# Kernel optimization log

Hardware: AMD Instinct MI355X
Metric: run time of the kernel (lower is better)

## Reference

```python
import jax, jax.numpy as jnp
import numpy as np

B, S, A, H, E = 8192, 256, 64, 1024, 8
IN = S + A
OUT = S + 1


def setup_inputs() -> dict:
    key = jax.random.key(0)
    ks = jax.random.split(key, 8)
    state = jax.random.normal(ks[0], (B, S), dtype=jnp.float32)
    action = jax.random.normal(ks[1], (B, A), dtype=jnp.float32)
    idx = jax.random.randint(ks[2], (B,), 0, E, dtype=jnp.int32)
    # Kaiming-ish scaling to keep activations sane
    W1 = jax.random.normal(ks[3], (E, IN, H), dtype=jnp.float32) / np.sqrt(IN)
    b1 = jnp.zeros((E, H), dtype=jnp.float32)
    W2 = jax.random.normal(ks[4], (E, H, H), dtype=jnp.float32) / np.sqrt(H)
    b2 = jnp.zeros((E, H), dtype=jnp.float32)
    W3 = jax.random.normal(ks[5], (E, H, OUT), dtype=jnp.float32) / np.sqrt(H)
    b3 = jnp.zeros((E, OUT), dtype=jnp.float32)
    return {"state": state, "action": action, "idx": idx,
            "W1": W1, "b1": b1, "W2": W2, "b2": b2, "W3": W3, "b3": b3}


def reference(state, action, idx, W1, b1, W2, b2, W3, b3):
    # Dense-MoE style: run all E experts on the full batch, then select the
    # per-sample expert output chosen by idx (matches masked gather/scatter
    # in the torch predict loop).
    x = jnp.concatenate([state, action], axis=-1)                  # [B, IN]
    h = jax.nn.relu(jnp.einsum('bi,eih->beh', x, W1) + b1)         # [B, E, H]
    h = jax.nn.relu(jnp.einsum('beh,ehk->bek', h, W2) + b2)        # [B, E, H]
    out = jnp.einsum('beh,eho->beo', h, W3) + b3                   # [B, E, S+1]
    sel = jnp.take_along_axis(out, idx[:, None, None], axis=1)[:, 0]  # [B, S+1]
    s_dim = state.shape[-1]
    delta = sel[:, :s_dim]
    reward = sel[:, s_dim:]
    next_state = state + delta
    return next_state, reward
```

## Files before the change

### kernel.cpp

```cpp
#include <hip/hip_runtime.h>
#include <stdint.h>

#define B_SZ   8192
#define IN_DIM 320
#define H_DIM  1024
#define E_NUM  8
#define OUT_DIM 257
#define TM     128
#define MAXT   (B_SZ / TM + E_NUM)

typedef __bf16 bf16x8 __attribute__((ext_vector_type(8)));
typedef float  f32x4  __attribute__((ext_vector_type(4)));

typedef unsigned int __attribute__((address_space(1))) as1_uint;
typedef unsigned int __attribute__((address_space(3))) as3_uint;

__device__ __forceinline__ void gload_lds16(const void* g, void* l) {
    __builtin_amdgcn_global_load_lds((const as1_uint*)g, (as3_uint*)l, 16, 0, 0);
}

__device__ __forceinline__ unsigned short f2bf(float f) {
    unsigned int u = __float_as_uint(f);
    return (unsigned short)((u + 0x7fffu + ((u >> 16) & 1u)) >> 16);
}

__global__ __launch_bounds__(256)
void k_prep(const float* __restrict__ state, const float* __restrict__ action,
            const int* __restrict__ idx,
            const float* __restrict__ W1, const float* __restrict__ W2,
            const float* __restrict__ W3,
            unsigned short* __restrict__ xb, unsigned short* __restrict__ w1t,
            unsigned short* __restrict__ w2t, unsigned short* __restrict__ w3t,
            int* __restrict__ order, int* __restrict__ te,
            int* __restrict__ tp0, int* __restrict__ tcnt) {
    __shared__ unsigned short tileU[64][65];
    __shared__ int scnt[16][E_NUM];
    int bid = blockIdx.x, tid = threadIdx.x;

    if (bid == 0) {
        int shard = tid & 15;
        if (tid < 128) ((int*)scnt)[tid] = 0;
        __syncthreads();
        for (int b = tid; b < B_SZ; b += 256) atomicAdd(&scnt[shard][idx[b]], 1);
        __syncthreads();
        if (tid == 0) {
            int pos = 0, tt = 0;
            for (int e = 0; e < E_NUM; e++) {
                int start = pos;
                for (int s = 0; s < 16; s++) { int c = scnt[s][e]; scnt[s][e] = pos; pos += c; }
                int tot = pos - start;
                for (int st = 0; st < tot; st += TM) {
                    te[tt] = e; tp0[tt] = start + st; tcnt[tt] = min(TM, tot - st); tt++;
                }
            }
            for (; tt < MAXT; tt++) { te[tt] = 0; tp0[tt] = 0; tcnt[tt] = 0; }
        }
        __syncthreads();
        for (int b = tid; b < B_SZ; b += 256) {
            int e = idx[b];
            int p = atomicAdd(&scnt[shard][e], 1);
            order[p] = b;
        }
        return;
    }

    if (bid <= 2560) {
        int q = (bid - 1) * 256 + tid;
        int b = q / 80, j = q % 80;
        float4 v = (j < 64) ? ((const float4*)state)[b * 64 + j]
                            : ((const float4*)action)[b * 16 + (j - 64)];
        ushort4 o;
        o.x = f2bf(v.x); o.y = f2bf(v.y); o.z = f2bf(v.z); o.w = f2bf(v.w);
        ((ushort4*)xb)[q] = o;
        return;
    }

    if (bid < 5761) {
        int e, kt, nt, K, Nsrc, dstRows; bool vec;
        const float* src; unsigned short* dst;
        if (bid < 3201) {
            int r = bid - 2561; e = r / 80; int m = r % 80; kt = m / 16; nt = m % 16;
            K = IN_DIM; Nsrc = H_DIM; dstRows = H_DIM; src = W1; dst = w1t; vec = true;
        } else if (bid < 5249) {
            int r = bid - 3201; e = r / 256; int m = r % 256; kt = m / 16; nt = m % 16;
            K = H_DIM; Nsrc = H_DIM; dstRows = H_DIM; src = W2; dst = w2t; vec = true;
        } else {
            int r = bid - 5249; e = r / 64; int m = r % 64; kt = m / 4; nt = m % 4;
            K = H_DIM; Nsrc = OUT_DIM; dstRows = 320; src = W3; dst = w3t; vec = false;
        }
        int k0 = kt * 64, n0 = nt * 64;
        const float* s = src + (size_t)e * K * Nsrc;
        unsigned short* d = dst + (size_t)e * dstRows * K;
        int c4 = (tid & 15) * 4;
        int rb = tid >> 4;

#pragma unroll
        for (int p = 0; p < 4; p++) {
            int r = rb + p * 16;
            const float* sp = s + (size_t)(k0 + r) * Nsrc + n0 + c4;
            float4 v;
            if (vec) v = *(const float4*)sp;
            else { v.x = sp[0]; v.y = sp[1]; v.z = sp[2]; v.w = sp[3]; }
            tileU[r][c4 + 0] = f2bf(v.x);
            tileU[r][c4 + 1] = f2bf(v.y);
            tileU[r][c4 + 2] = f2bf(v.z);
            tileU[r][c4 + 3] = f2bf(v.w);
        }
        __syncthreads();
#pragma unroll
        for (int p = 0; p < 4; p++) {
            int n = rb + p * 16;
            ushort4 o;
            o.x = tileU[c4 + 0][n];
            o.y = tileU[c4 + 1][n];
            o.z = tileU[c4 + 2][n];
            o.w = tileU[c4 + 3][n];
            *(ushort4*)&d[(size_t)(n0 + n) * K + k0 + c4] = o;
        }
        return;
    }

    int i = (bid - 5761) * 256 + tid;
    int e = i >> 10, k = i & 1023;
    w3t[((size_t)e * 320 + 256) * H_DIM + k] =
        f2bf(W3[((size_t)e * H_DIM + k) * OUT_DIM + 256]);
}

template <int K, int TN, bool GATHER, int MODE>
__global__ __launch_bounds__(256, 2)
void k_gemm(const unsigned short* __restrict__ Abase,
            const unsigned short* __restrict__ Wt, int wtRows,
            const float* __restrict__ bias, int bstride,
            unsigned short* __restrict__ Hout,
            float* __restrict__ Out, const float* __restrict__ state,
            const int* __restrict__ order,
            const int* __restrict__ te, const int* __restrict__ tp0,
            const int* __restrict__ tcnt) {
    constexpr int NI  = K / 32;
    constexpr int WN  = TN / 2;
    constexpr int NF  = WN / 16;
    constexpr int ABY = 128 * 64;
    constexpr int BBY = TN * 64;
    constexpr int STG = ABY + BBY;
    constexpr int BL  = TN / 64;
    __shared__ __align__(16) char lds[2 * STG];

    int t = blockIdx.x;
    int cnt = tcnt[t];
    if (cnt == 0) return;
    int e = te[t], p0 = tp0[t];
    int n0 = blockIdx.y * TN;
    int tid = threadIdx.x;
    int w = tid >> 6, lane = tid & 63;
    int wm = w >> 1, wn = w & 1;

    int r0 = tid >> 2;
    int cg = (tid & 3) ^ ((r0 >> 1) & 3);
    int rc0 = r0 < cnt ? r0 : cnt - 1;
    int rc1 = (r0 + 64) < cnt ? (r0 + 64) : cnt - 1;
    long a0 = GATHER ? order[p0 + rc0] : (p0 + rc0);
    long a1 = GATHER ? order[p0 + rc1] : (p0 + rc1);
    const unsigned short* aP0 = Abase + (size_t)a0 * K + cg * 8;
    const unsigned short* aP1 = Abase + (size_t)a1 * K + cg * 8;
    const unsigned short* bP0 = Wt + ((size_t)e * wtRows + n0 + r0) * K + cg * 8;
    const unsigned short* bP1 = bP0 + (size_t)64 * K;

    auto stage = [&](int k0, int sb) {
        gload_lds16(aP0 + k0, lds + sb + tid * 16);
        gload_lds16(aP1 + k0, lds + sb + 4096 + tid * 16);
        gload_lds16(bP0 + k0, lds + sb + ABY + tid * 16);
        if (BL == 2)
            gload_lds16(bP1 + k0, lds + sb + ABY + 4096 + tid * 16);
    };

    f32x4 acc[4][NF];
#pragma unroll
    for (int i = 0; i < 4; i++)
#pragma unroll
        for (int j = 0; j < NF; j++) acc[i][j] = (f32x4)0.f;

    const int fm   = lane & 15;
    const int kc   = lane >> 4;
    const int koff = ((kc ^ ((fm >> 1) & 3)) * 8);

    stage(0, 0);
    for (int it = 0; it < NI; ++it) {
        __syncthreads();
        if (it + 1 < NI) stage((it + 1) * 32, ((it + 1) & 1) * STG);
        const unsigned short* Ls = (const unsigned short*)(lds + (it & 1) * STG);
        const unsigned short* As = Ls + wm * 64 * 32;
        const unsigned short* Bs = Ls + ABY / 2 + wn * WN * 32;

        bf16x8 af[4], bf[NF];
#pragma unroll
        for (int i = 0; i < 4; i++)
            af[i] = *(const bf16x8*)&As[(i * 16 + fm) * 32 + koff];
#pragma unroll
        for (int j = 0; j < NF; j++)
            bf[j] = *(const bf16x8*)&Bs[(j * 16 + fm) * 32 + koff];
#pragma unroll
        for (int i = 0; i < 4; i++)
#pragma unroll
            for (int j = 0; j < NF; j++)
                acc[i][j] = __builtin_amdgcn_mfma_f32_16x16x32_bf16(
                    af[i], bf[j], acc[i][j], 0, 0, 0);
    }

    int col = lane & 15, rq = lane >> 4;
#pragma unroll
    for (int j = 0; j < NF; j++) {
        int n = n0 + wn * WN + j * 16 + col;
        float bv = (MODE == 0) ? bias[e * bstride + n]
                               : ((n <= 256) ? bias[e * bstride + n] : 0.f);
#pragma unroll
        for (int i = 0; i < 4; i++) {
#pragma unroll
            for (int rr = 0; rr < 4; rr++) {
                int m = wm * 64 + i * 16 + rq * 4 + rr;
                if (m < cnt) {
                    float v = acc[i][j][rr] + bv;
                    if (MODE == 0) {
                        Hout[(size_t)(p0 + m) * H_DIM + n] = f2bf(fmaxf(v, 0.f));
                    } else {
                        int row = order[p0 + m];
                        if (n < 256) {
                            size_t o = (size_t)row * 256 + n;
                            Out[o] = state[o] + v;
                        } else if (n == 256) {
                            Out[(size_t)B_SZ * 256 + row] = v;
                        }
                    }
                }
            }
        }
    }
}

extern "C" void kernel_launch(void* const* d_in, const int* in_sizes, int n_in,
                              void* d_out, int out_size, void* d_ws, size_t ws_size,
                              hipStream_t stream) {
    const float* state  = (const float*)d_in[0];
    const float* action = (const float*)d_in[1];
    const int*   idx    = (const int*)d_in[2];
    const float* W1     = (const float*)d_in[3];
    const float* b1     = (const float*)d_in[4];
    const float* W2     = (const float*)d_in[5];
    const float* b2     = (const float*)d_in[6];
    const float* W3     = (const float*)d_in[7];
    const float* b3     = (const float*)d_in[8];
    float* out = (float*)d_out;

    char* ws = (char*)d_ws;
    size_t off = 0;
    auto alloc = [&](size_t bytes) -> void* {
        void* p = ws + off;
        off = (off + bytes + 255) & ~(size_t)255;
        return p;
    };
    unsigned short* xb  = (unsigned short*)alloc((size_t)B_SZ * IN_DIM * 2);
    unsigned short* w1t = (unsigned short*)alloc((size_t)E_NUM * H_DIM * IN_DIM * 2);
    unsigned short* w2t = (unsigned short*)alloc((size_t)E_NUM * H_DIM * H_DIM * 2);
    unsigned short* w3t = (unsigned short*)alloc((size_t)E_NUM * 320 * H_DIM * 2);
    unsigned short* h1  = (unsigned short*)alloc((size_t)B_SZ * H_DIM * 2);
    unsigned short* h2  = (unsigned short*)alloc((size_t)B_SZ * H_DIM * 2);
    int* order = (int*)alloc(B_SZ * 4);
    int* te    = (int*)alloc(MAXT * 4);
    int* tp0   = (int*)alloc(MAXT * 4);
    int* tcnt  = (int*)alloc(MAXT * 4);

    k_prep<<<5793, 256, 0, stream>>>(state, action, idx, W1, W2, W3,
                                     xb, w1t, w2t, w3t, order, te, tp0, tcnt);

    k_gemm<IN_DIM, 128, true, 0><<<dim3(MAXT, 8), 256, 0, stream>>>(
        xb, w1t, H_DIM, b1, H_DIM, h1, nullptr, nullptr, order, te, tp0, tcnt);
    k_gemm<H_DIM, 128, false, 0><<<dim3(MAXT, 8), 256, 0, stream>>>(
        h1, w2t, H_DIM, b2, H_DIM, h2, nullptr, nullptr, order, te, tp0, tcnt);
    k_gemm<H_DIM, 64, false, 1><<<dim3(MAXT, 5), 256, 0, stream>>>(
        h2, w3t, 320, b3, OUT_DIM, nullptr, out, state, order, te, tp0, tcnt);
}
```

Measured before the change: 227.6 us.

## Use smaller GEMM tiles for layers 1 and 3; register-transpose weight prep

Templates the grouped GEMM on the M tile size. Layer 1 moves to 64-wide N tiles, which doubles its block count. Layer 3 moves to 64x64 tiles driven by a second per-expert tile list that k_prep now builds, to raise parallelism on the narrow output GEMM. The weight conversion kernel drops the LDS-staged transpose and does a 4x4 transpose in registers per thread, which removes a barrier and the shared memory but makes the global reads strided across lanes.

```diff
diff --git a/kernel.cpp b/kernel.cpp
--- a/kernel.cpp
+++ b/kernel.cpp
@@ -6,11 +6,12 @@
 #define H_DIM  1024
 #define E_NUM  8
 #define OUT_DIM 257
-#define TM     128
-#define MAXT   (B_SZ / TM + E_NUM)
+#define MAXT1  (B_SZ / 128 + E_NUM)
+#define MAXT2  (B_SZ / 64 + E_NUM)
 
 typedef __bf16 bf16x8 __attribute__((ext_vector_type(8)));
 typedef float  f32x4  __attribute__((ext_vector_type(4)));
+typedef float  f32x4v __attribute__((ext_vector_type(4)));
 
 typedef unsigned int __attribute__((address_space(1))) as1_uint;
 typedef unsigned int __attribute__((address_space(3))) as3_uint;
@@ -31,9 +32,9 @@
             const float* __restrict__ W3,
             unsigned short* __restrict__ xb, unsigned short* __restrict__ w1t,
             unsigned short* __restrict__ w2t, unsigned short* __restrict__ w3t,
-            int* __restrict__ order, int* __restrict__ te,
-            int* __restrict__ tp0, int* __restrict__ tcnt) {
-    __shared__ unsigned short tileU[64][65];
+            int* __restrict__ order,
+            int* __restrict__ te,  int* __restrict__ tp0, int* __restrict__ tcnt,
+            int* __restrict__ te2, int* __restrict__ tp2, int* __restrict__ tc2) {
     __shared__ int scnt[16][E_NUM];
     int bid = blockIdx.x, tid = threadIdx.x;
 
@@ -44,16 +45,20 @@
         for (int b = tid; b < B_SZ; b += 256) atomicAdd(&scnt[shard][idx[b]], 1);
         __syncthreads();
         if (tid == 0) {
-            int pos = 0, tt = 0;
+            int pos = 0, t1 = 0, t2 = 0;
             for (int e = 0; e < E_NUM; e++) {
                 int start = pos;
                 for (int s = 0; s < 16; s++) { int c = scnt[s][e]; scnt[s][e] = pos; pos += c; }
                 int tot = pos - start;
-                for (int st = 0; st < tot; st += TM) {
-                    te[tt] = e; tp0[tt] = start + st; tcnt[tt] = min(TM, tot - st); tt++;
+                for (int st = 0; st < tot; st += 128) {
+                    te[t1] = e; tp0[t1] = start + st; tcnt[t1] = min(128, tot - st); t1++;
+                }
+                for (int st = 0; st < tot; st += 64) {
+                    te2[t2] = e; tp2[t2] = start + st; tc2[t2] = min(64, tot - st); t2++;
                 }
             }
-            for (; tt < MAXT; tt++) { te[tt] = 0; tp0[tt] = 0; tcnt[tt] = 0; }
+            for (; t1 < MAXT1; t1++) { te[t1] = 0; tp0[t1] = 0; tcnt[t1] = 0; }
+            for (; t2 < MAXT2; t2++) { te2[t2] = 0; tp2[t2] = 0; tc2[t2] = 0; }
         }
         __syncthreads();
         for (int b = tid; b < B_SZ; b += 256) {
@@ -91,31 +96,27 @@
         int k0 = kt * 64, n0 = nt * 64;
         const float* s = src + (size_t)e * K * Nsrc;
         unsigned short* d = dst + (size_t)e * dstRows * K;
-        int c4 = (tid & 15) * 4;
-        int rb = tid >> 4;
-
-#pragma unroll
-        for (int p = 0; p < 4; p++) {
-            int r = rb + p * 16;
-            const float* sp = s + (size_t)(k0 + r) * Nsrc + n0 + c4;
-            float4 v;
-            if (vec) v = *(const float4*)sp;
-            else { v.x = sp[0]; v.y = sp[1]; v.z = sp[2]; v.w = sp[3]; }
-            tileU[r][c4 + 0] = f2bf(v.x);
-            tileU[r][c4 + 1] = f2bf(v.y);
-            tileU[r][c4 + 2] = f2bf(v.z);
-            tileU[r][c4 + 3] = f2bf(v.w);
-        }
-        __syncthreads();
-#pragma unroll
-        for (int p = 0; p < 4; p++) {
-            int n = rb + p * 16;
+        int kc4 = (tid & 15) * 4;
+        int nc4 = (tid >> 4) * 4;
+        const float* sp = s + (size_t)(k0 + kc4) * Nsrc + n0 + nc4;
+        f32x4v v[4];
+        if (vec) {
+#pragma unroll
+            for (int i = 0; i < 4; i++)
+                v[i] = *(const f32x4v*)(sp + (size_t)i * Nsrc);
+        } else {
+#pragma unroll
+            for (int i = 0; i < 4; i++)
+#pragma unroll
+                for (int j = 0; j < 4; j++)
+                    v[i][j] = sp[(size_t)i * Nsrc + j];
+        }
+#pragma unroll
+        for (int j = 0; j < 4; j++) {
             ushort4 o;
-            o.x = tileU[c4 + 0][n];
-            o.y = tileU[c4 + 1][n];
-            o.z = tileU[c4 + 2][n];
-            o.w = tileU[c4 + 3][n];
-            *(ushort4*)&d[(size_t)(n0 + n) * K + k0 + c4] = o;
+            o.x = f2bf(v[0][j]); o.y = f2bf(v[1][j]);
+            o.z = f2bf(v[2][j]); o.w = f2bf(v[3][j]);
+            *(ushort4*)&d[(size_t)(n0 + nc4 + j) * K + k0 + kc4] = o;
         }
         return;
     }
@@ -126,7 +127,7 @@
         f2bf(W3[((size_t)e * H_DIM + k) * OUT_DIM + 256]);
 }
 
-template <int K, int TN, bool GATHER, int MODE>
+template <int K, int TM, int TN, bool GATHER, int MODE>
 __global__ __launch_bounds__(256, 2)
 void k_gemm(const unsigned short* __restrict__ Abase,
             const unsigned short* __restrict__ Wt, int wtRows,
@@ -137,12 +138,11 @@
             const int* __restrict__ te, const int* __restrict__ tp0,
             const int* __restrict__ tcnt) {
     constexpr int NI  = K / 32;
-    constexpr int WN  = TN / 2;
-    constexpr int NF  = WN / 16;
-    constexpr int ABY = 128 * 64;
+    constexpr int WM  = TM / 2, MF = WM / 16;
+    constexpr int WN  = TN / 2, NF = WN / 16;
+    constexpr int ABY = TM * 64;
     constexpr int BBY = TN * 64;
     constexpr int STG = ABY + BBY;
-    constexpr int BL  = TN / 64;
     __shared__ __align__(16) char lds[2 * STG];
 
     int t = blockIdx.x;
@@ -157,25 +157,29 @@
     int r0 = tid >> 2;
     int cg = (tid & 3) ^ ((r0 >> 1) & 3);
     int rc0 = r0 < cnt ? r0 : cnt - 1;
-    int rc1 = (r0 + 64) < cnt ? (r0 + 64) : cnt - 1;
     long a0 = GATHER ? order[p0 + rc0] : (p0 + rc0);
-    long a1 = GATHER ? order[p0 + rc1] : (p0 + rc1);
     const unsigned short* aP0 = Abase + (size_t)a0 * K + cg * 8;
-    const unsigned short* aP1 = Abase + (size_t)a1 * K + cg * 8;
+    const unsigned short* aP1 = aP0;
+    if (TM == 128) {
+        int rc1 = (r0 + 64) < cnt ? (r0 + 64) : cnt - 1;
+        long a1 = GATHER ? order[p0 + rc1] : (p0 + rc1);
+        aP1 = Abase + (size_t)a1 * K + cg * 8;
+    }
     const unsigned short* bP0 = Wt + ((size_t)e * wtRows + n0 + r0) * K + cg * 8;
     const unsigned short* bP1 = bP0 + (size_t)64 * K;
 
-    auto stage = [&](int k0, int sb) {
-        gload_lds16(aP0 + k0, lds + sb + tid * 16);
-        gload_lds16(aP1 + k0, lds + sb + 4096 + tid * 16);
-        gload_lds16(bP0 + k0, lds + sb + ABY + tid * 16);
-        if (BL == 2)
-            gload_lds16(bP1 + k0, lds + sb + ABY + 4096 + tid * 16);
+    auto stage = [&](int k0s, int sb) {
+        gload_lds16(aP0 + k0s, lds + sb + tid * 16);
+        if (TM == 128)
+            gload_lds16(aP1 + k0s, lds + sb + 4096 + tid * 16);
+        gload_lds16(bP0 + k0s, lds + sb + ABY + tid * 16);
+        if (TN == 128)
+            gload_lds16(bP1 + k0s, lds + sb + ABY + 4096 + tid * 16);
     };
 
-    f32x4 acc[4][NF];
-#pragma unroll
-    for (int i = 0; i < 4; i++)
+    f32x4 acc[MF][NF];
+#pragma unroll
+    for (int i = 0; i < MF; i++)
 #pragma unroll
         for (int j = 0; j < NF; j++) acc[i][j] = (f32x4)0.f;
 
@@ -188,18 +192,18 @@
         __syncthreads();
         if (it + 1 < NI) stage((it + 1) * 32, ((it + 1) & 1) * STG);
         const unsigned short* Ls = (const unsigned short*)(lds + (it & 1) * STG);
-        const unsigned short* As = Ls + wm * 64 * 32;
+        const unsigned short* As = Ls + wm * WM * 32;
         const unsigned short* Bs = Ls + ABY / 2 + wn * WN * 32;
 
-        bf16x8 af[4], bf[NF];
-#pragma unroll
-        for (int i = 0; i < 4; i++)
+        bf16x8 af[MF], bf[NF];
+#pragma unroll
+        for (int i = 0; i < MF; i++)
             af[i] = *(const bf16x8*)&As[(i * 16 + fm) * 32 + koff];
 #pragma unroll
         for (int j = 0; j < NF; j++)
             bf[j] = *(const bf16x8*)&Bs[(j * 16 + fm) * 32 + koff];
 #pragma unroll
-        for (int i = 0; i < 4; i++)
+        for (int i = 0; i < MF; i++)
 #pragma unroll
             for (int j = 0; j < NF; j++)
                 acc[i][j] = __builtin_amdgcn_mfma_f32_16x16x32_bf16(
@@ -213,10 +217,10 @@
         float bv = (MODE == 0) ? bias[e * bstride + n]
                                : ((n <= 256) ? bias[e * bstride + n] : 0.f);
 #pragma unroll
-        for (int i = 0; i < 4; i++) {
+        for (int i = 0; i < MF; i++) {
 #pragma unroll
             for (int rr = 0; rr < 4; rr++) {
-                int m = wm * 64 + i * 16 + rq * 4 + rr;
+                int m = wm * WM + i * 16 + rq * 4 + rr;
                 if (m < cnt) {
                     float v = acc[i][j][rr] + bv;
                     if (MODE == 0) {
@@ -264,17 +268,21 @@
     unsigned short* h1  = (unsigned short*)alloc((size_t)B_SZ * H_DIM * 2);
     unsigned short* h2  = (unsigned short*)alloc((size_t)B_SZ * H_DIM * 2);
     int* order = (int*)alloc(B_SZ * 4);
-    int* te    = (int*)alloc(MAXT * 4);
-    int* tp0   = (int*)alloc(MAXT * 4);
-    int* tcnt  = (int*)alloc(MAXT * 4);
+    int* te    = (int*)alloc(MAXT1 * 4);
+    int* tp0   = (int*)alloc(MAXT1 * 4);
+    int* tcnt  = (int*)alloc(MAXT1 * 4);
+    int* te2   = (int*)alloc(MAXT2 * 4);
+    int* tp2   = (int*)alloc(MAXT2 * 4);
+    int* tc2   = (int*)alloc(MAXT2 * 4);
 
     k_prep<<<5793, 256, 0, stream>>>(state, action, idx, W1, W2, W3,
-                                     xb, w1t, w2t, w3t, order, te, tp0, tcnt);
-
-    k_gemm<IN_DIM, 128, true, 0><<<dim3(MAXT, 8), 256, 0, stream>>>(
+                                     xb, w1t, w2t, w3t, order,
+                                     te, tp0, tcnt, te2, tp2, tc2);
+
+    k_gemm<IN_DIM, 128, 64, true, 0><<<dim3(MAXT1, 16), 256, 0, stream>>>(
         xb, w1t, H_DIM, b1, H_DIM, h1, nullptr, nullptr, order, te, tp0, tcnt);
-    k_gemm<H_DIM, 128, false, 0><<<dim3(MAXT, 8), 256, 0, stream>>>(
+    k_gemm<H_DIM, 128, 128, false, 0><<<dim3(MAXT1, 8), 256, 0, stream>>>(
         h1, w2t, H_DIM, b2, H_DIM, h2, nullptr, nullptr, order, te, tp0, tcnt);
-    k_gemm<H_DIM, 64, false, 1><<<dim3(MAXT, 5), 256, 0, stream>>>(
-        h2, w3t, 320, b3, OUT_DIM, nullptr, out, state, order, te, tp0, tcnt);
-}
+    k_gemm<H_DIM, 64, 64, false, 1><<<dim3(MAXT2, 5), 256, 0, stream>>>(
+        h2, w3t, 320, b3, OUT_DIM, nullptr, out, state, order, te2, tp2, tc2);
+}
```

Result: no change. 229.8 us (+0.9%).
